# Optimization experiments

Measured on AMD Instinct MI355X. Metric: run time of the kernel, lower is better.

Reference implementation:

```python
import jax, jax.numpy as jnp
import numpy as np

SLOTS = 64
TOPK = 1
GATE_MAX = 0.2
MEM_SCALE = 0.5
DELTA_CLIP = 2.0
LN_EPS = 1e-5


def setup_inputs() -> dict:
    key = jax.random.key(0)
    ks = jax.random.split(key, 6)
    B, T, D = 8, 4096, 896
    h = jax.random.normal(ks[0], (B, T, D), dtype=jnp.float32)
    attention_mask = jnp.ones((B, T), dtype=jnp.int32)
    ln_g = jnp.ones((D,), dtype=jnp.float32)
    ln_b = jnp.zeros((D,), dtype=jnp.float32)
    W_out = (jax.random.normal(ks[1], (D, D), dtype=jnp.float32) * 0.02)      # mem_out: Linear(D,D,bias=False)
    W_nm = (jax.random.normal(ks[2], (1, 2 * D), dtype=jnp.float32) * 0.02)   # neuromod: Linear(2D,1)
    b_nm = jnp.zeros((1,), dtype=jnp.float32)
    W_wg = (jax.random.normal(ks[3], (1, D + 1), dtype=jnp.float32) * 0.02)   # write_gate: Linear(D+1,1)
    b_wg = jnp.zeros((1,), dtype=jnp.float32)
    return dict(h=h, attention_mask=attention_mask, ln_g=ln_g, ln_b=ln_b,
                W_out=W_out, W_nm=W_nm, b_nm=b_nm, W_wg=W_wg, b_wg=b_wg)


def reference(h, attention_mask, ln_g, ln_b, W_out, W_nm, b_nm, W_wg, b_wg):
    B, T, D = h.shape
    scale = 1.0 / jnp.sqrt(jnp.float32(D))
    mem_k0 = jnp.zeros((B, SLOTS, D), dtype=jnp.float32)
    mem_v0 = jnp.zeros((B, SLOTS, D), dtype=jnp.float32)
    keep = attention_mask.astype(jnp.float32)
    batch_idx = jnp.arange(B)[:, None]

    def step(carry, xs):
        mem_k, mem_v = carry
        h_t, keep_t = xs                                   # [B,D], [B]
        # content-based read: attention over slots
        scores = jnp.einsum('bd,bsd->bs', h_t, mem_k) * scale
        attn = jax.nn.softmax(scores, axis=-1)
        m = jnp.einsum('bs,bsd->bd', attn, mem_v)          # [B,D]
        # neuromodulator gate
        g = jax.nn.sigmoid(jnp.concatenate([h_t, m], axis=-1) @ W_nm.T + b_nm)   # [B,1]
        # write gate, clamped and masked by attention mask
        wg = jax.nn.sigmoid(jnp.concatenate([h_t, g], axis=-1) @ W_wg.T + b_wg)  # [B,1]
        wg = jnp.clip(wg, 0.0, GATE_MAX) * keep_t[:, None]
        # top-k gated write with straight-through selection
        soft = jax.nn.softmax(scores, axis=-1)             # address by content similarity
        _, idx = jax.lax.top_k(soft, TOPK)                 # [B,TOPK]
        hard = jnp.zeros_like(soft).at[batch_idx, idx].set(1.0 / TOPK)
        w = hard + soft - jax.lax.stop_gradient(soft)      # straight-through weights [B,S]
        gw = (wg * w)[..., None]                           # [B,S,1]
        mem_k = mem_k * (1.0 - gw) + gw * h_t[:, None, :]
        mem_v = mem_v * (1.0 - gw) + gw * h_t[:, None, :]
        # memory residual: LN -> Linear -> scale -> clip
        mu = jnp.mean(m, axis=-1, keepdims=True)
        var = jnp.var(m, axis=-1, keepdims=True)
        mn = (m - mu) / jnp.sqrt(var + LN_EPS) * ln_g + ln_b
        delta = jnp.clip((mn @ W_out.T) * MEM_SCALE, -DELTA_CLIP, DELTA_CLIP)
        return (mem_k, mem_v), h_t + delta

    xs = (jnp.swapaxes(h, 0, 1), jnp.swapaxes(keep, 0, 1))  # time-major for scan
    (_, _), h2 = jax.lax.scan(step, (mem_k0, mem_v0), xs)
    return jnp.swapaxes(h2, 0, 1)                          # [B,T,D]
```

## Files before the change

### kernel.cpp

```cpp
#include <hip/hip_runtime.h>
#include <hip/hip_bf16.h>

#define DIM 896
#define TT 4096
#define BB 8
#define NS 64
#define CC 128
#define NC 32
#define RCH 256
#define NRC 16
#define NSLICE 14

typedef float floatx4 __attribute__((ext_vector_type(4)));
typedef short short8 __attribute__((ext_vector_type(8)));

#define DPP_F(x_, ctrl_, rmask_, old_) \
  __int_as_float(__builtin_amdgcn_update_dpp(__float_as_int(old_), __float_as_int(x_), (ctrl_), (rmask_), 0xf, false))

__device__ __forceinline__ float wave_sum64(float x) {
    x += DPP_F(x, 0x111, 0xf, 0.0f);
    x += DPP_F(x, 0x112, 0xf, 0.0f);
    x += DPP_F(x, 0x114, 0xf, 0.0f);
    x += DPP_F(x, 0x118, 0xf, 0.0f);
    x += DPP_F(x, 0x142, 0xa, 0.0f);
    x += DPP_F(x, 0x143, 0xc, 0.0f);
    return __int_as_float(__builtin_amdgcn_readlane(__float_as_int(x), 63));
}
__device__ __forceinline__ float wave_max64(float x) {
    x = fmaxf(x, DPP_F(x, 0x111, 0xf, -INFINITY));
    x = fmaxf(x, DPP_F(x, 0x112, 0xf, -INFINITY));
    x = fmaxf(x, DPP_F(x, 0x114, 0xf, -INFINITY));
    x = fmaxf(x, DPP_F(x, 0x118, 0xf, -INFINITY));
    x = fmaxf(x, DPP_F(x, 0x142, 0xa, -INFINITY));
    x = fmaxf(x, DPP_F(x, 0x143, 0xc, -INFINITY));
    return __int_as_float(__builtin_amdgcn_readlane(__float_as_int(x), 63));
}

__device__ __forceinline__ float rfl_f(float x) {
    return __int_as_float(__builtin_amdgcn_readfirstlane(__float_as_int(x)));
}
__device__ __forceinline__ float rl_f(float x, int l) {
    return __int_as_float(__builtin_amdgcn_readlane(__float_as_int(x), l));
}

__global__ __launch_bounds__(64) void k0_dots(const float* __restrict__ h,
                                              const float* __restrict__ W_nm,
                                              const float* __restrict__ W_wg,
                                              float* __restrict__ R, float* __restrict__ Q,
                                              float* __restrict__ P2) {
    const int r = blockIdx.x;
    const int lane = threadIdx.x;
    const float2* hr = (const float2*)(h + (size_t)r * DIM);
    const float2* w0 = (const float2*)W_nm;
    const float2* w1 = (const float2*)(W_nm + DIM);
    const float2* w2 = (const float2*)W_wg;
    float a = 0.f, bsum = 0.f, c = 0.f;
    #pragma unroll
    for (int i = 0; i < 7; ++i) {
        int idx = lane + 64 * i;
        float2 hv = hr[idx];
        float2 a0 = w0[idx], a1 = w1[idx], a2 = w2[idx];
        a = fmaf(hv.x, a0.x, fmaf(hv.y, a0.y, a));
        bsum = fmaf(hv.x, a1.x, fmaf(hv.y, a1.y, bsum));
        c = fmaf(hv.x, a2.x, fmaf(hv.y, a2.y, c));
    }
    #pragma unroll
    for (int off = 32; off; off >>= 1) {
        a += __shfl_xor(a, off);
        bsum += __shfl_xor(bsum, off);
        c += __shfl_xor(c, off);
    }
    if (lane == 0) { R[r] = a; P2[r] = bsum; Q[r] = c; }
}

__global__ __launch_bounds__(256) void kG_gram(const float* __restrict__ h,
                                               float* __restrict__ Gd) {
    const int blk = blockIdx.x;
    const int bc = blk >> 1, half = blk & 1;
    const int b = bc / NC, c = bc % NC;
    const int tid = threadIdx.x;
    const int ti = tid >> 4, tj = tid & 15;
    __shared__ float Hs[32][132];
    float acc[8][4];
    #pragma unroll
    for (int u = 0; u < 8; u++)
        #pragma unroll
        for (int v = 0; v < 4; v++) acc[u][v] = 0.f;
    const size_t hb = (size_t)b * TT * DIM + (size_t)c * CC * DIM;
    for (int kb = 0; kb < 28; ++kb) {
        __syncthreads();
        #pragma unroll
        for (int l = 0; l < 4; ++l) {
            int idx = tid + l * 256;
            int r = idx >> 3, kq = idx & 7;
            float4 f = *(const float4*)&h[hb + (size_t)r * DIM + kb * 32 + kq * 4];
            Hs[kq * 4 + 0][r] = f.x; Hs[kq * 4 + 1][r] = f.y;
            Hs[kq * 4 + 2][r] = f.z; Hs[kq * 4 + 3][r] = f.w;
        }
        __syncthreads();
        #pragma unroll 4
        for (int k = 0; k < 32; ++k) {
            float4 a0 = *(const float4*)&Hs[k][ti * 8];
            float4 a1 = *(const float4*)&Hs[k][ti * 8 + 4];
            float4 bv = *(const float4*)&Hs[k][half * 64 + tj * 4];
            float av[8] = {a0.x, a0.y, a0.z, a0.w, a1.x, a1.y, a1.z, a1.w};
            float bb[4] = {bv.x, bv.y, bv.z, bv.w};
            #pragma unroll
            for (int u = 0; u < 8; u++)
                #pragma unroll
                for (int v = 0; v < 4; v++)
                    acc[u][v] = fmaf(av[u], bb[v], acc[u][v]);
        }
    }
    float* gp = Gd + (size_t)bc * CC * CC;
    #pragma unroll
    for (int u = 0; u < 8; u++) {
        float4 o = {acc[u][0], acc[u][1], acc[u][2], acc[u][3]};
        *(float4*)&gp[(size_t)(ti * 8 + u) * CC + half * 64 + tj * 4] = o;
    }
}

#define MC_(i) case i: mc[i] = fmaf(mc[i], om, wh); break;
__global__ __launch_bounds__(256) void kB_base(const float* __restrict__ h,
                                               const float* __restrict__ wgbuf,
                                               const int* __restrict__ ssbuf,
                                               float* __restrict__ memS,
                                               float* __restrict__ snap,
                                               float* __restrict__ Bpart,
                                               int c) {
    const int slice = blockIdx.x;
    const int b = blockIdx.y;
    const int tid = threadIdx.x;
    __shared__ float wsh[CC];
    __shared__ int   ssh[CC];
    __shared__ float Asb[64][65];
    __shared__ float Bsb[CC][65];

    if (tid < CC) {
        wsh[tid] = wgbuf[b * TT + (c - 1) * CC + tid];
        ssh[tid] = ssbuf[b * TT + (c - 1) * CC + tid];
    }
    const int q = tid >> 6, d = tid & 63;
    const int dg = slice * 64 + d;
    float mc[16];
    #pragma unroll
    for (int j = 0; j < 16; j++) mc[j] = memS[((size_t)b * NS + q * 16 + j) * DIM + dg];
    __syncthreads();

    const size_t hb = (size_t)b * TT * DIM + (size_t)((c - 1) * CC) * DIM + dg;
    float hv[16];
    #pragma unroll
    for (int j = 0; j < 16; ++j) hv[j] = h[hb + (size_t)j * DIM];
    for (int i0 = 0; i0 < CC; i0 += 16) {
        float hvn[16];
        if (i0 + 16 < CC) {
            #pragma unroll
            for (int j = 0; j < 16; ++j) hvn[j] = h[hb + (size_t)(i0 + 16 + j) * DIM];
        }
        #pragma unroll
        for (int j = 0; j < 16; ++j) {
            const int i = i0 + j;
            float hvv = hv[j];
            int ss = __builtin_amdgcn_readfirstlane(ssh[i]);
            float w = rfl_f(wsh[i]);
            if ((ss >> 4) == q) {
                float om = 1.f - w, wh = w * hvv;
                switch (ss & 15) {
                    MC_(0) MC_(1) MC_(2) MC_(3) MC_(4) MC_(5) MC_(6) MC_(7)
                    MC_(8) MC_(9) MC_(10) MC_(11) MC_(12) MC_(13) MC_(14) MC_(15)
                }
            }
        }
        #pragma unroll
        for (int j = 0; j < 16; ++j) hv[j] = hvn[j];
    }
    #pragma unroll
    for (int j = 0; j < 16; j++) {
        memS[((size_t)b * NS + q * 16 + j) * DIM + dg] = mc[j];
        Asb[d][q * 16 + j] = mc[j];
    }
    if ((c & 1) == 0) {
        const int r = c >> 1;
        #pragma unroll
        for (int j = 0; j < 16; j++)
            snap[(((size_t)b * NRC + r) * NS + q * 16 + j) * DIM + dg] = mc[j];
    }
    const size_t hb2 = (size_t)b * TT * DIM + (size_t)(c * CC) * DIM + slice * 64;
    for (int idx = tid; idx < CC * 64; idx += 256) {
        int tp = idx >> 6, k = idx & 63;
        Bsb[tp][k] = h[hb2 + (size_t)tp * DIM + k];
    }
    __syncthreads();

    const int tg = tid >> 3, sg = tid & 7;
    float acc[4][8];
    #pragma unroll
    for (int v = 0; v < 4; v++)
        #pragma unroll
        for (int u = 0; u < 8; u++) acc[v][u] = 0.f;
    #pragma unroll 4
    for (int k = 0; k < 64; ++k) {
        float bv[4], av[8];
        #pragma unroll
        for (int v = 0; v < 4; v++) bv[v] = Bsb[tg * 4 + v][k];
        #pragma unroll
        for (int u = 0; u < 8; u++) av[u] = Asb[k][sg * 8 + u];
        #pragma unroll
        for (int v = 0; v < 4; v++)
            #pragma unroll
            for (int u = 0; u < 8; u++)
                acc[v][u] = fmaf(bv[v], av[u], acc[v][u]);
    }
    float* bp = Bpart + ((size_t)(slice * BB + b)) * CC * NS;
    #pragma unroll
    for (int v = 0; v < 4; v++) {
        float4 o0 = {acc[v][0], acc[v][1], acc[v][2], acc[v][3]};
        float4 o1 = {acc[v][4], acc[v][5], acc[v][6], acc[v][7]};
        *(float4*)&bp[(size_t)(tg * 4 + v) * NS + sg * 8] = o0;
        *(float4*)&bp[(size_t)(tg * 4 + v) * NS + sg * 8 + 4] = o1;
    }
}

__global__ __launch_bounds__(256) void kS_seq(const float* __restrict__ Bpart,
                                              const float* __restrict__ Gd,
                                              const float* __restrict__ Rv,
                                              const float* __restrict__ Qv,
                                              const float* __restrict__ P2v,
                                              const int* __restrict__ mask,
                                              const float* __restrict__ b_nm,
                                              const float* __restrict__ b_wg,
                                              const float* __restrict__ W_wg,
                                              float* __restrict__ Kvec,
                                              float* __restrict__ fbuf,
                                              float* __restrict__ wgbuf,
                                              int* __restrict__ ssbuf,
                                              int c) {
    const int b = blockIdx.x;
    const int tid = threadIdx.x;
    const int lane = tid & 63;
    __shared__ float S[CC * 65];
    const int t0 = c * CC;
    const int tb = b * TT + t0;

    {
        const int w4 = tid >> 6;
        if (c == 0) {
            #pragma unroll 4
            for (int t = w4 * 32; t < w4 * 32 + 32; ++t) S[t * 65 + lane] = 0.f;
        } else {
            const float* bp0 = Bpart + (size_t)b * CC * NS;
            for (int t = w4 * 32; t < w4 * 32 + 32; ++t) {
                float s = 0.f;
                #pragma unroll
                for (int sl = 0; sl < NSLICE; ++sl)
                    s += bp0[(size_t)sl * (BB * CC * NS) + (size_t)t * NS + lane];
                S[t * 65 + lane] = s;
            }
        }
    }
    __syncthreads();
    if (tid >= 64) return;

    float Rl0 = Rv[tb + lane],  Rl1 = Rv[tb + 64 + lane];
    float Ql0 = Qv[tb + lane],  Ql1 = Qv[tb + 64 + lane];
    float Pl0 = P2v[tb + lane], Pl1 = P2v[tb + 64 + lane];
    float Ml0 = (float)mask[tb + lane], Ml1 = (float)mask[tb + 64 + lane];

    float K = Kvec[b * NS + lane];
    const float scale = 1.0f / sqrtf((float)DIM);
    const float bnm = b_nm[0], bwg = b_wg[0], wD = W_wg[DIM];
    const float* gdc = Gd + (size_t)(b * NC + c) * CC * CC;

    float g0s[4], g1s[4];
    #pragma unroll
    for (int j = 0; j < 4; ++j) {
        int r1 = j + 1 + lane, r2 = j + 65 + lane;
        g0s[j] = gdc[(size_t)j * CC + r1];
        g1s[j] = (r2 < CC) ? gdc[(size_t)j * CC + r2] : 0.f;
    }
    float cur = S[0 * 65 + lane];
    float p1 = S[1 * 65 + lane];
    float p2 = S[2 * 65 + lane];
    float p3 = S[3 * 65 + lane];

    for (int T = 0; T < CC; T += 4) {
        #pragma unroll
        for (int j = 0; j < 4; ++j) {
            const int tau = T + j;
            float p4 = (tau + 4 < CC) ? S[(tau + 4) * 65 + lane] : 0.f;
            const float g0 = g0s[j], g1 = g1s[j];
            {
                const int tn = tau + 4;
                int r1n = tn + 1 + lane, r2n = tn + 65 + lane;
                g0s[j] = (tn < CC && r1n < CC) ? gdc[(size_t)tn * CC + r1n] : 0.f;
                g1s[j] = (tn < CC && r2n < CC) ? gdc[(size_t)tn * CC + r2n] : 0.f;
            }
            const float Rt = rl_f((tau & 64) ? Rl1 : Rl0, tau & 63);
            const float Qt = rl_f((tau & 64) ? Ql1 : Ql0, tau & 63);
            const float Pt = rl_f((tau & 64) ? Pl1 : Pl0, tau & 63);
            const float Mk = rl_f((tau & 64) ? Ml1 : Ml0, tau & 63);

            float sco = cur * scale;
            float mv = wave_max64(sco);
            float e = __expf(sco);
            float se = wave_sum64(e);
            float sk = wave_sum64(e * K);
            unsigned long long bal = __ballot(sco == mv);
            int mi = (int)__ffsll(bal) - 1;

            float inv = 1.f / se;
            fbuf[((size_t)tb + tau) * NS + lane] = e * inv;
            float gdot = sk * inv;
            float g = 1.f / (1.f + __expf(-(Rt + gdot + bnm)));
            float w = 1.f / (1.f + __expf(-(Qt + g * wD + bwg)));
            w = fminf(w, 0.2f) * Mk;
            if (lane == 0) {
                wgbuf[tb + tau] = w;
                ssbuf[tb + tau] = mi;
            }
            float om = 1.f - w;
            K = (lane == mi) ? fmaf(K, om, w * Pt) : K;

            int r1 = tau + 1 + lane, r2 = tau + 65 + lane;
            if (lane >= 4 && r1 < CC) S[r1 * 65 + mi] = fmaf(S[r1 * 65 + mi], om, w * g0);
            if (r2 < CC) S[r2 * 65 + mi] = fmaf(S[r2 * 65 + mi], om, w * g1);

            const float q1 = rl_f(g0, 0), q2 = rl_f(g0, 1);
            const float q3 = rl_f(g0, 2), q4 = rl_f(g0, 3);
            const bool m_ = (lane == mi);
            p1 = m_ ? fmaf(p1, om, w * q1) : p1;
            p2 = m_ ? fmaf(p2, om, w * q2) : p2;
            p3 = m_ ? fmaf(p3, om, w * q3) : p3;
            p4 = m_ ? fmaf(p4, om, w * q4) : p4;
            cur = p1; p1 = p2; p2 = p3; p3 = p4;
        }
    }
    Kvec[b * NS + lane] = K;
}

__global__ __launch_bounds__(256) void k1_wcvt(const float* __restrict__ W,
                                               __hip_bfloat16* __restrict__ Wb) {
    const int idx = blockIdx.x * 256 + threadIdx.x;
    const float4 f = ((const float4*)W)[idx];
    alignas(8) __hip_bfloat16 t[4];
    t[0] = __float2bfloat16(f.x); t[1] = __float2bfloat16(f.y);
    t[2] = __float2bfloat16(f.z); t[3] = __float2bfloat16(f.w);
    *(uint2*)&Wb[(size_t)idx * 4] = *(const uint2*)t;
}

#define CS_(i) case i: mem[i] = fmaf(mem[i], sA, aB); break;
__global__ __launch_bounds__(448) void k2_replay(const float* __restrict__ h,
                                                 const float* __restrict__ fbuf,
                                                 const float* __restrict__ wgbuf,
                                                 const int* __restrict__ ssbuf,
                                                 const float* __restrict__ snap,
                                                 __hip_bfloat16* __restrict__ Mbuf) {
    const int blk = blockIdx.x;
    const int b = blk >> 5;
    const int c = (blk >> 1) & 15;
    const int halfD = blk & 1;
    const int tid = threadIdx.x;
    const int dg = halfD * 448 + tid;

    __shared__ float lf[128 * NS];
    __shared__ float lwg[RCH];
    __shared__ int   lss[RCH];

    float mem[64];
    const float* sp = snap + (((size_t)b * NRC + c) * NS) * DIM + dg;
    #pragma unroll
    for (int s2 = 0; s2 < 64; s2++) mem[s2] = sp[(size_t)s2 * DIM];

    const int t0 = c * RCH;
    if (tid < RCH) {
        lwg[tid] = wgbuf[b * TT + t0 + tid];
        lss[tid] = ssbuf[b * TT + t0 + tid];
    }
    const size_t hbase = (size_t)b * TT * DIM + (size_t)t0 * DIM + dg;
    const size_t fbase = ((size_t)b * TT + t0) * NS;
    const size_t mrow = ((size_t)b * TT + t0) * DIM + dg;

    for (int half = 0; half < 2; ++half) {
        __syncthreads();
        const float4* src = (const float4*)(fbuf + fbase + (size_t)half * 128 * NS);
        for (int idx = tid; idx < 128 * NS / 4; idx += 448)
            ((float4*)lf)[idx] = src[idx];
        __syncthreads();

        float hv[8];
        #pragma unroll
        for (int j = 0; j < 8; ++j)
            hv[j] = h[hbase + (size_t)(half * 128 + j) * DIM];

        for (int tg = 0; tg < 128; tg += 8) {
            float hvn[8];
            if (tg + 8 < 128) {
                #pragma unroll
                for (int j = 0; j < 8; ++j)
                    hvn[j] = h[hbase + (size_t)(half * 128 + tg + 8 + j) * DIM];
            }
// ... 19 lines not shown
                    CS_(0) CS_(1) CS_(2) CS_(3) CS_(4) CS_(5) CS_(6) CS_(7)
                    CS_(8) CS_(9) CS_(10) CS_(11) CS_(12) CS_(13) CS_(14) CS_(15)
                    CS_(16) CS_(17) CS_(18) CS_(19) CS_(20) CS_(21) CS_(22) CS_(23)
                    CS_(24) CS_(25) CS_(26) CS_(27) CS_(28) CS_(29) CS_(30) CS_(31)
                    CS_(32) CS_(33) CS_(34) CS_(35) CS_(36) CS_(37) CS_(38) CS_(39)
                    CS_(40) CS_(41) CS_(42) CS_(43) CS_(44) CS_(45) CS_(46) CS_(47)
                    CS_(48) CS_(49) CS_(50) CS_(51) CS_(52) CS_(53) CS_(54) CS_(55)
                    CS_(56) CS_(57) CS_(58) CS_(59) CS_(60) CS_(61) CS_(62) CS_(63)
                }
            }
            #pragma unroll
            for (int j = 0; j < 8; ++j) hv[j] = hvn[j];
        }
    }
}

__global__ __launch_bounds__(64) void k3_ln(__hip_bfloat16* __restrict__ Mbuf,
                                            const float* __restrict__ ln_g,
                                            const float* __restrict__ ln_b) {
    const size_t r = blockIdx.x;
    const int lane = threadIdx.x;
    __hip_bfloat162* row2 = (__hip_bfloat162*)(Mbuf + r * DIM);
    float vx[7], vy[7];
    float s1 = 0.f, s2 = 0.f;
    #pragma unroll
    for (int i = 0; i < 7; i++) {
        __hip_bfloat162 x2 = row2[lane + 64 * i];
        float x = __bfloat162float(x2.x), y = __bfloat162float(x2.y);
        vx[i] = x; vy[i] = y;
        s1 += x + y;
        s2 = fmaf(x, x, fmaf(y, y, s2));
    }
    #pragma unroll
    for (int off = 32; off; off >>= 1) {
        s1 += __shfl_xor(s1, off);
        s2 += __shfl_xor(s2, off);
    }
    float mu = s1 * (1.0f / DIM);
    float var = fmaxf(s2 * (1.0f / DIM) - mu * mu, 0.0f);
    float rs = 1.0f / sqrtf(var + 1e-5f);
    #pragma unroll
    for (int i = 0; i < 7; i++) {
        int d = 2 * (lane + 64 * i);
        float2 lg = *(const float2*)&ln_g[d];
        float2 lb = *(const float2*)&ln_b[d];
        __hip_bfloat162 o;
        o.x = __float2bfloat16((vx[i] - mu) * rs * lg.x + lb.x);
        o.y = __float2bfloat16((vy[i] - mu) * rs * lg.y + lb.y);
        row2[lane + 64 * i] = o;
    }
}

__global__ __launch_bounds__(256) void k4_gemm(const __hip_bfloat16* __restrict__ Mn,
                                               const __hip_bfloat16* __restrict__ Wb,
                                               const float* __restrict__ h,
                                               float* __restrict__ out) {
    const int nt = blockIdx.x;
    const int mt = blockIdx.y;
    const int tid = threadIdx.x;
    const int wave = tid >> 6, lane = tid & 63;
    const int wr = wave >> 1, wc = wave & 1;

    __shared__ __hip_bfloat16 Asb[128 * 72];
    __shared__ __hip_bfloat16 Bsb[128 * 72];

    floatx4 acc[4][4];
    #pragma unroll
    for (int i = 0; i < 4; i++)
        #pragma unroll
        for (int jn = 0; jn < 4; jn++)
            acc[i][jn] = (floatx4){0.f, 0.f, 0.f, 0.f};

    const int lrow = lane & 15;
    const int lk = (lane >> 4) * 8;
    const int rr = tid >> 3, ch = tid & 7;

    for (int kt = 0; kt < 14; ++kt) {
        #pragma unroll
        for (int it = 0; it < 4; ++it) {
            int row = rr + 32 * it;
            const uint4* srcA = (const uint4*)(Mn + ((size_t)(mt * 128 + row)) * DIM + kt * 64 + ch * 8);
            *(uint4*)&Asb[row * 72 + ch * 8] = *srcA;
            const uint4* srcB = (const uint4*)(Wb + ((size_t)(nt * 128 + row)) * DIM + kt * 64 + ch * 8);
            *(uint4*)&Bsb[row * 72 + ch * 8] = *srcB;
        }
        __syncthreads();
        #pragma unroll
        for (int kk = 0; kk < 2; ++kk) {
            short8 af[4], bfr[4];
            #pragma unroll
            for (int i = 0; i < 4; i++)
                af[i] = *(const short8*)&Asb[(wr * 64 + i * 16 + lrow) * 72 + kk * 32 + lk];
            #pragma unroll
            for (int i2 = 0; i2 < 4; i2++)
                bfr[i2] = *(const short8*)&Bsb[(wc * 64 + i2 * 16 + lrow) * 72 + kk * 32 + lk];
            #pragma unroll
            for (int i = 0; i < 4; i++)
                #pragma unroll
                for (int jn = 0; jn < 4; jn++)
                    acc[i][jn] = __builtin_amdgcn_mfma_f32_16x16x32_bf16(af[i], bfr[jn], acc[i][jn], 0, 0, 0);
        }
        __syncthreads();
    }
    const int crow = (lane >> 4) * 4, ccol = lane & 15;
    #pragma unroll
    for (int i = 0; i < 4; i++)
        #pragma unroll
        for (int jn = 0; jn < 4; jn++)
            #pragma unroll
            for (int rg = 0; rg < 4; rg++) {
                int rG = mt * 128 + wr * 64 + i * 16 + crow + rg;
                int nG = nt * 128 + wc * 64 + jn * 16 + ccol;
                size_t idx = (size_t)rG * DIM + nG;
                float d = acc[i][jn][rg] * 0.5f;
                d = fminf(fmaxf(d, -2.0f), 2.0f);
                out[idx] = h[idx] + d;
            }
}

extern "C" void kernel_launch(void* const* d_in, const int* in_sizes, int n_in,
                              void* d_out, int out_size, void* d_ws, size_t ws_size,
                              hipStream_t stream) {
    const float* h      = (const float*)d_in[0];
    const int* mask     = (const int*)d_in[1];
    const float* ln_g   = (const float*)d_in[2];
    const float* ln_b   = (const float*)d_in[3];
    const float* W_out  = (const float*)d_in[4];
    const float* W_nm   = (const float*)d_in[5];
    const float* b_nm   = (const float*)d_in[6];
    const float* W_wg   = (const float*)d_in[7];
    const float* b_wg   = (const float*)d_in[8];
    float* out = (float*)d_out;

    char* ws = (char*)d_ws;
    float* Bpart = (float*)(ws);
    float* memS  = (float*)(ws + 8388608);
    float* Kvec  = (float*)(ws + 8388608 + 1835008);
    float* snap  = (float*)(ws + 8388608 + 1835008 + 2048);
    const size_t Z0 = 8388608;
    const size_t ZBYTES = 1835008 + 2048 + 29360128;
    float* fbuf  = (float*)(ws + 8388608 + ZBYTES);
    float* wgbuf = (float*)(ws + 8388608 + ZBYTES + 8388608);
    int*   ssbuf = (int*)  (ws + 8388608 + ZBYTES + 8388608 + 131072);
    char*  Mreg  = ws + 8388608 + ZBYTES + 8388608 + 262144;
    float* Gd = (float*)(Mreg);
    float* R  = (float*)(Mreg + 16777216);
    float* Q  = (float*)(Mreg + 16777216 + 131072);
    float* P2 = (float*)(Mreg + 16777216 + 262144);
    __hip_bfloat16* Mbuf = (__hip_bfloat16*)Mreg;
    __hip_bfloat16* Wb = (__hip_bfloat16*)(ws);

    hipMemsetAsync(ws + Z0, 0, ZBYTES, stream);
    hipLaunchKernelGGL(k0_dots, dim3(BB * TT), dim3(64), 0, stream,
                       h, W_nm, W_wg, R, Q, P2);
    hipLaunchKernelGGL(kG_gram, dim3(BB * NC * 2), dim3(256), 0, stream, h, Gd);

    hipLaunchKernelGGL(kS_seq, dim3(BB), dim3(256), 0, stream,
                       Bpart, Gd, R, Q, P2, mask, b_nm, b_wg, W_wg,
                       Kvec, fbuf, wgbuf, ssbuf, 0);
    for (int c = 1; c < NC; ++c) {
        hipLaunchKernelGGL(kB_base, dim3(NSLICE, BB), dim3(256), 0, stream,
                           h, wgbuf, ssbuf, memS, snap, Bpart, c);
        hipLaunchKernelGGL(kS_seq, dim3(BB), dim3(256), 0, stream,
                           Bpart, Gd, R, Q, P2, mask, b_nm, b_wg, W_wg,
                           Kvec, fbuf, wgbuf, ssbuf, c);
    }

    hipLaunchKernelGGL(k1_wcvt, dim3(784), dim3(256), 0, stream, W_out, Wb);
    hipLaunchKernelGGL(k2_replay, dim3(BB * NRC * 2), dim3(448), 0, stream,
                       h, fbuf, wgbuf, ssbuf, snap, Mbuf);
    hipLaunchKernelGGL(k3_ln, dim3(BB * TT), dim3(64), 0, stream,
                       Mbuf, ln_g, ln_b);
    hipLaunchKernelGGL(k4_gemm, dim3(7, 256), dim3(256), 0, stream,
                       Mbuf, Wb, h, out);
}
```

Baseline: 4.320 ms.

## Double chunk size to halve sequential launches and fold weight conversion into GEMM

Raises the chunk length from 128 to 256 steps, halving the number of serialized kB_base/kS_seq launch pairs. The Gram kernel now computes the 256x256 per-chunk Gram from three 128x128 tiles (the symmetric lower block is skipped) and uses a skewed shared-memory layout. The sequential kernel keeps four register-carried rows and holds a larger S array in shared memory, so each kS_seq call does twice the serial work. The separate W_out bf16 conversion kernel is removed and the conversion happens inside the GEMM tile load instead, which repeats the conversion work across blocks.

```diff
diff --git a/kernel.cpp b/kernel.cpp
--- a/kernel.cpp
+++ b/kernel.cpp
@@ -5,8 +5,8 @@
 #define TT 4096
 #define BB 8
 #define NS 64
-#define CC 128
-#define NC 32
+#define CC 256
+#define NC 16
 #define RCH 256
 #define NRC 16
 #define NSLICE 14
@@ -73,50 +73,69 @@
     if (lane == 0) { R[r] = a; P2[r] = bsum; Q[r] = c; }
 }
 
+#define KSW(cx) ((cx) + (((cx) >> 5) << 2))
 __global__ __launch_bounds__(256) void kG_gram(const float* __restrict__ h,
                                                float* __restrict__ Gd) {
     const int blk = blockIdx.x;
-    const int bc = blk >> 1, half = blk & 1;
+    const int bc = blk / 3, pair = blk % 3;
     const int b = bc / NC, c = bc % NC;
+    const int rh = (pair == 2) ? 1 : 0;
+    const int ch2 = (pair >= 1) ? 1 : 0;
     const int tid = threadIdx.x;
     const int ti = tid >> 4, tj = tid & 15;
-    __shared__ float Hs[32][132];
-    float acc[8][4];
+    __shared__ float Ar[32 * 140];
+    __shared__ float Ac[32 * 140];
+    float acc[8][8];
     #pragma unroll
     for (int u = 0; u < 8; u++)
         #pragma unroll
-        for (int v = 0; v < 4; v++) acc[u][v] = 0.f;
-    const size_t hb = (size_t)b * TT * DIM + (size_t)c * CC * DIM;
+        for (int v = 0; v < 8; v++) acc[u][v] = 0.f;
+    const size_t hbR = (size_t)b * TT * DIM + (size_t)(c * CC + rh * 128) * DIM;
+    const size_t hbC = (size_t)b * TT * DIM + (size_t)(c * CC + ch2 * 128) * DIM;
+    const float* Acp = (pair == 1) ? Ac : Ar;
+    const int cbr = ti * 8 + ((ti >> 2) << 2);
+    const int cbc = tj * 8 + ((tj >> 2) << 2);
     for (int kb = 0; kb < 28; ++kb) {
         __syncthreads();
         #pragma unroll
         for (int l = 0; l < 4; ++l) {
             int idx = tid + l * 256;
             int r = idx >> 3, kq = idx & 7;
-            float4 f = *(const float4*)&h[hb + (size_t)r * DIM + kb * 32 + kq * 4];
-            Hs[kq * 4 + 0][r] = f.x; Hs[kq * 4 + 1][r] = f.y;
-            Hs[kq * 4 + 2][r] = f.z; Hs[kq * 4 + 3][r] = f.w;
+            int rs = KSW(r);
+            float4 f = *(const float4*)&h[hbR + (size_t)r * DIM + kb * 32 + kq * 4];
+            Ar[(kq * 4 + 0) * 140 + rs] = f.x; Ar[(kq * 4 + 1) * 140 + rs] = f.y;
+            Ar[(kq * 4 + 2) * 140 + rs] = f.z; Ar[(kq * 4 + 3) * 140 + rs] = f.w;
+            if (pair == 1) {
+                float4 g = *(const float4*)&h[hbC + (size_t)r * DIM + kb * 32 + kq * 4];
+                Ac[(kq * 4 + 0) * 140 + rs] = g.x; Ac[(kq * 4 + 1) * 140 + rs] = g.y;
+                Ac[(kq * 4 + 2) * 140 + rs] = g.z; Ac[(kq * 4 + 3) * 140 + rs] = g.w;
+            }
         }
         __syncthreads();
         #pragma unroll 4
         for (int k = 0; k < 32; ++k) {
-            float4 a0 = *(const float4*)&Hs[k][ti * 8];
-            float4 a1 = *(const float4*)&Hs[k][ti * 8 + 4];
-            float4 bv = *(const float4*)&Hs[k][half * 64 + tj * 4];
+            float4 a0 = *(const float4*)&Ar[k * 140 + cbr];
+            float4 a1 = *(const float4*)&Ar[k * 140 + cbr + 4];
+            float4 b0 = *(const float4*)&Acp[k * 140 + cbc];
+            float4 b1 = *(const float4*)&Acp[k * 140 + cbc + 4];
             float av[8] = {a0.x, a0.y, a0.z, a0.w, a1.x, a1.y, a1.z, a1.w};
-            float bb[4] = {bv.x, bv.y, bv.z, bv.w};
+            float bv[8] = {b0.x, b0.y, b0.z, b0.w, b1.x, b1.y, b1.z, b1.w};
             #pragma unroll
             for (int u = 0; u < 8; u++)
                 #pragma unroll
-                for (int v = 0; v < 4; v++)
-                    acc[u][v] = fmaf(av[u], bb[v], acc[u][v]);
+                for (int v = 0; v < 8; v++)
+                    acc[u][v] = fmaf(av[u], bv[v], acc[u][v]);
         }
     }
     float* gp = Gd + (size_t)bc * CC * CC;
     #pragma unroll
     for (int u = 0; u < 8; u++) {
-        float4 o = {acc[u][0], acc[u][1], acc[u][2], acc[u][3]};
-        *(float4*)&gp[(size_t)(ti * 8 + u) * CC + half * 64 + tj * 4] = o;
+        int row = rh * 128 + ti * 8 + u;
+        int col = ch2 * 128 + tj * 8;
+        float4 o0 = {acc[u][0], acc[u][1], acc[u][2], acc[u][3]};
+        float4 o1 = {acc[u][4], acc[u][5], acc[u][6], acc[u][7]};
+        *(float4*)&gp[(size_t)row * CC + col] = o0;
+        *(float4*)&gp[(size_t)row * CC + col + 4] = o1;
     }
 }
 
@@ -134,12 +153,10 @@
     __shared__ float wsh[CC];
     __shared__ int   ssh[CC];
     __shared__ float Asb[64][65];
-    __shared__ float Bsb[CC][65];
-
-    if (tid < CC) {
-        wsh[tid] = wgbuf[b * TT + (c - 1) * CC + tid];
-        ssh[tid] = ssbuf[b * TT + (c - 1) * CC + tid];
-    }
+    __shared__ float Bsb[128][65];
+
+    wsh[tid] = wgbuf[b * TT + (c - 1) * CC + tid];
+    ssh[tid] = ssbuf[b * TT + (c - 1) * CC + tid];
     const int q = tid >> 6, d = tid & 63;
     const int dg = slice * 64 + d;
     float mc[16];
@@ -179,45 +196,45 @@
         memS[((size_t)b * NS + q * 16 + j) * DIM + dg] = mc[j];
         Asb[d][q * 16 + j] = mc[j];
     }
-    if ((c & 1) == 0) {
-        const int r = c >> 1;
-        #pragma unroll
-        for (int j = 0; j < 16; j++)
-            snap[(((size_t)b * NRC + r) * NS + q * 16 + j) * DIM + dg] = mc[j];
-    }
-    const size_t hb2 = (size_t)b * TT * DIM + (size_t)(c * CC) * DIM + slice * 64;
-    for (int idx = tid; idx < CC * 64; idx += 256) {
-        int tp = idx >> 6, k = idx & 63;
-        Bsb[tp][k] = h[hb2 + (size_t)tp * DIM + k];
-    }
-    __syncthreads();
+    #pragma unroll
+    for (int j = 0; j < 16; j++)
+        snap[(((size_t)b * NRC + c) * NS + q * 16 + j) * DIM + dg] = mc[j];
 
     const int tg = tid >> 3, sg = tid & 7;
-    float acc[4][8];
-    #pragma unroll
-    for (int v = 0; v < 4; v++)
-        #pragma unroll
-        for (int u = 0; u < 8; u++) acc[v][u] = 0.f;
-    #pragma unroll 4
-    for (int k = 0; k < 64; ++k) {
-        float bv[4], av[8];
-        #pragma unroll
-        for (int v = 0; v < 4; v++) bv[v] = Bsb[tg * 4 + v][k];
-        #pragma unroll
-        for (int u = 0; u < 8; u++) av[u] = Asb[k][sg * 8 + u];
+    float* bp = Bpart + ((size_t)(slice * BB + b)) * CC * NS;
+    for (int hf = 0; hf < 2; ++hf) {
+        __syncthreads();
+        const size_t hb2 = (size_t)b * TT * DIM + (size_t)(c * CC + hf * 128) * DIM + slice * 64;
+        for (int idx = tid; idx < 128 * 64; idx += 256) {
+            int tp = idx >> 6, k = idx & 63;
+            Bsb[tp][k] = h[hb2 + (size_t)tp * DIM + k];
+        }
+        __syncthreads();
+        float acc[4][8];
         #pragma unroll
         for (int v = 0; v < 4; v++)
             #pragma unroll
-            for (int u = 0; u < 8; u++)
-                acc[v][u] = fmaf(bv[v], av[u], acc[v][u]);
-    }
-    float* bp = Bpart + ((size_t)(slice * BB + b)) * CC * NS;
-    #pragma unroll
-    for (int v = 0; v < 4; v++) {
-        float4 o0 = {acc[v][0], acc[v][1], acc[v][2], acc[v][3]};
-        float4 o1 = {acc[v][4], acc[v][5], acc[v][6], acc[v][7]};
-        *(float4*)&bp[(size_t)(tg * 4 + v) * NS + sg * 8] = o0;
-        *(float4*)&bp[(size_t)(tg * 4 + v) * NS + sg * 8 + 4] = o1;
+            for (int u = 0; u < 8; u++) acc[v][u] = 0.f;
+        #pragma unroll 4
+        for (int k = 0; k < 64; ++k) {
+            float bv[4], av[8];
+            #pragma unroll
+            for (int v = 0; v < 4; v++) bv[v] = Bsb[tg * 4 + v][k];
+            #pragma unroll
+            for (int u = 0; u < 8; u++) av[u] = Asb[k][sg * 8 + u];
+            #pragma unroll
+            for (int v = 0; v < 4; v++)
+                #pragma unroll
+                for (int u = 0; u < 8; u++)
+                    acc[v][u] = fmaf(bv[v], av[u], acc[v][u]);
+        }
+        #pragma unroll
+        for (int v = 0; v < 4; v++) {
+            float4 o0 = {acc[v][0], acc[v][1], acc[v][2], acc[v][3]};
+            float4 o1 = {acc[v][4], acc[v][5], acc[v][6], acc[v][7]};
+            *(float4*)&bp[(size_t)(hf * 128 + tg * 4 + v) * NS + sg * 8] = o0;
+            *(float4*)&bp[(size_t)(hf * 128 + tg * 4 + v) * NS + sg * 8 + 4] = o1;
+        }
     }
 }
 
@@ -238,67 +255,94 @@
     const int b = blockIdx.x;
     const int tid = threadIdx.x;
     const int lane = tid & 63;
-    __shared__ float S[CC * 65];
+    __shared__ float S[252 * 65];
     const int t0 = c * CC;
     const int tb = b * TT + t0;
-
-    {
+    const float* bp0 = Bpart + (size_t)b * CC * NS;
+
+    if (c == 0) {
         const int w4 = tid >> 6;
-        if (c == 0) {
-            #pragma unroll 4
-            for (int t = w4 * 32; t < w4 * 32 + 32; ++t) S[t * 65 + lane] = 0.f;
-        } else {
-            const float* bp0 = Bpart + (size_t)b * CC * NS;
-            for (int t = w4 * 32; t < w4 * 32 + 32; ++t) {
-                float s = 0.f;
-                #pragma unroll
-                for (int sl = 0; sl < NSLICE; ++sl)
-                    s += bp0[(size_t)sl * (BB * CC * NS) + (size_t)t * NS + lane];
-                S[t * 65 + lane] = s;
-            }
+        for (int t = 4 + w4 * 63; t < 4 + w4 * 63 + 63 && t < 256; ++t) S[(t - 4) * 65 + lane] = 0.f;
+        for (int t = 4 + 252 + tid; t < 256; t += 256) S[(t - 4) * 65 + lane] = 0.f;
+    } else {
+        const int quad = tid & 15;
+        const int g16 = tid >> 4;
+        for (int t = 4 + g16; t < 256; t += 16) {
+            float s0 = 0.f, s1 = 0.f, s2 = 0.f, s3 = 0.f;
+            #pragma unroll
+            for (int sl = 0; sl < NSLICE; ++sl) {
+                float4 v = *(const float4*)&bp0[(size_t)sl * (BB * CC * NS) + (size_t)t * NS + quad * 4];
+                s0 += v.x; s1 += v.y; s2 += v.z; s3 += v.w;
+            }
+            S[(t - 4) * 65 + quad * 4 + 0] = s0;
+            S[(t - 4) * 65 + quad * 4 + 1] = s1;
+            S[(t - 4) * 65 + quad * 4 + 2] = s2;
+            S[(t - 4) * 65 + quad * 4 + 3] = s3;
         }
     }
     __syncthreads();
     if (tid >= 64) return;
 
-    float Rl0 = Rv[tb + lane],  Rl1 = Rv[tb + 64 + lane];
-    float Ql0 = Qv[tb + lane],  Ql1 = Qv[tb + 64 + lane];
-    float Pl0 = P2v[tb + lane], Pl1 = P2v[tb + 64 + lane];
-    float Ml0 = (float)mask[tb + lane], Ml1 = (float)mask[tb + 64 + lane];
+    float cur, p1, p2, p3;
+    if (c == 0) { cur = p1 = p2 = p3 = 0.f; }
+    else {
+        float c0 = 0.f, c1 = 0.f, c2 = 0.f, c3 = 0.f;
+        #pragma unroll
+        for (int sl = 0; sl < NSLICE; ++sl) {
+            const float* p = bp0 + (size_t)sl * (BB * CC * NS);
+            c0 += p[lane]; c1 += p[64 + lane]; c2 += p[128 + lane]; c3 += p[192 + lane];
+        }
+        cur = c0; p1 = c1; p2 = c2; p3 = c3;
+    }
+
+    float Rl0 = Rv[tb + lane],       Rl1 = Rv[tb + 64 + lane];
+    float Rl2 = Rv[tb + 128 + lane], Rl3 = Rv[tb + 192 + lane];
+    float Ql0 = Qv[tb + lane],       Ql1 = Qv[tb + 64 + lane];
+    float Ql2 = Qv[tb + 128 + lane], Ql3 = Qv[tb + 192 + lane];
+    float Pl0 = P2v[tb + lane],      Pl1 = P2v[tb + 64 + lane];
+    float Pl2 = P2v[tb + 128 + lane],Pl3 = P2v[tb + 192 + lane];
+    float Ml0 = (float)mask[tb + lane],       Ml1 = (float)mask[tb + 64 + lane];
+    float Ml2 = (float)mask[tb + 128 + lane], Ml3 = (float)mask[tb + 192 + lane];
 
     float K = Kvec[b * NS + lane];
     const float scale = 1.0f / sqrtf((float)DIM);
     const float bnm = b_nm[0], bwg = b_wg[0], wD = W_wg[DIM];
     const float* gdc = Gd + (size_t)(b * NC + c) * CC * CC;
 
-    float g0s[4], g1s[4];
+    float g0s[4], g1s[4], g2s[4], g3s[4];
     #pragma unroll
     for (int j = 0; j < 4; ++j) {
-        int r1 = j + 1 + lane, r2 = j + 65 + lane;
+        int r1 = j + 1 + lane, r2 = j + 65 + lane, r3 = j + 129 + lane, r4 = j + 193 + lane;
         g0s[j] = gdc[(size_t)j * CC + r1];
-        g1s[j] = (r2 < CC) ? gdc[(size_t)j * CC + r2] : 0.f;
-    }
-    float cur = S[0 * 65 + lane];
-    float p1 = S[1 * 65 + lane];
-    float p2 = S[2 * 65 + lane];
-    float p3 = S[3 * 65 + lane];
+        g1s[j] = gdc[(size_t)j * CC + r2];
+        g2s[j] = gdc[(size_t)j * CC + r3];
+        g3s[j] = (r4 < CC) ? gdc[(size_t)j * CC + r4] : 0.f;
+    }
 
     for (int T = 0; T < CC; T += 4) {
         #pragma unroll
         for (int j = 0; j < 4; ++j) {
             const int tau = T + j;
-            float p4 = (tau + 4 < CC) ? S[(tau + 4) * 65 + lane] : 0.f;
-            const float g0 = g0s[j], g1 = g1s[j];
+            float p4 = (tau + 4 < CC) ? S[tau * 65 + lane] : 0.f;
+            const float g0 = g0s[j], g1 = g1s[j], g2 = g2s[j], g3 = g3s[j];
             {
                 const int tn = tau + 4;
                 int r1n = tn + 1 + lane, r2n = tn + 65 + lane;
+                int r3n = tn + 129 + lane, r4n = tn + 193 + lane;
                 g0s[j] = (tn < CC && r1n < CC) ? gdc[(size_t)tn * CC + r1n] : 0.f;
                 g1s[j] = (tn < CC && r2n < CC) ? gdc[(size_t)tn * CC + r2n] : 0.f;
-            }
-            const float Rt = rl_f((tau & 64) ? Rl1 : Rl0, tau & 63);
-            const float Qt = rl_f((tau & 64) ? Ql1 : Ql0, tau & 63);
-            const float Pt = rl_f((tau & 64) ? Pl1 : Pl0, tau & 63);
-            const float Mk = rl_f((tau & 64) ? Ml1 : Ml0, tau & 63);
+                g2s[j] = (tn < CC && r3n < CC) ? gdc[(size_t)tn * CC + r3n] : 0.f;
+                g3s[j] = (tn < CC && r4n < CC) ? gdc[(size_t)tn * CC + r4n] : 0.f;
+            }
+            const int t6a = (tau >> 7) & 1, t6b = (tau >> 6) & 1;
+            float Rsel = t6a ? (t6b ? Rl3 : Rl2) : (t6b ? Rl1 : Rl0);
+            float Qsel = t6a ? (t6b ? Ql3 : Ql2) : (t6b ? Ql1 : Ql0);
+            float Psel = t6a ? (t6b ? Pl3 : Pl2) : (t6b ? Pl1 : Pl0);
+            float Msel = t6a ? (t6b ? Ml3 : Ml2) : (t6b ? Ml1 : Ml0);
+            const float Rt = rl_f(Rsel, tau & 63);
+            const float Qt = rl_f(Qsel, tau & 63);
+            const float Pt = rl_f(Psel, tau & 63);
+            const float Mk = rl_f(Msel, tau & 63);
 
             float sco = cur * scale;
             float mv = wave_max64(sco);
@@ -322,8 +366,11 @@
             K = (lane == mi) ? fmaf(K, om, w * Pt) : K;
 
             int r1 = tau + 1 + lane, r2 = tau + 65 + lane;
-            if (lane >= 4 && r1 < CC) S[r1 * 65 + mi] = fmaf(S[r1 * 65 + mi], om, w * g0);
-            if (r2 < CC) S[r2 * 65 + mi] = fmaf(S[r2 * 65 + mi], om, w * g1);
+            int r3 = tau + 129 + lane, r4 = tau + 193 + lane;
+            if (lane >= 4 && r1 < CC) S[(r1 - 4) * 65 + mi] = fmaf(S[(r1 - 4) * 65 + mi], om, w * g0);
+            if (r2 < CC) S[(r2 - 4) * 65 + mi] = fmaf(S[(r2 - 4) * 65 + mi], om, w * g1);
+            if (r3 < CC) S[(r3 - 4) * 65 + mi] = fmaf(S[(r3 - 4) * 65 + mi], om, w * g2);
+            if (r4 < CC) S[(r4 - 4) * 65 + mi] = fmaf(S[(r4 - 4) * 65 + mi], om, w * g3);
 
             const float q1 = rl_f(g0, 0), q2 = rl_f(g0, 1);
             const float q3 = rl_f(g0, 2), q4 = rl_f(g0, 3);
@@ -336,16 +383,6 @@
         }
     }
     Kvec[b * NS + lane] = K;
-}
-
-__global__ __launch_bounds__(256) void k1_wcvt(const float* __restrict__ W,
-                                               __hip_bfloat16* __restrict__ Wb) {
-    const int idx = blockIdx.x * 256 + threadIdx.x;
-    const float4 f = ((const float4*)W)[idx];
-    alignas(8) __hip_bfloat16 t[4];
-    t[0] = __float2bfloat16(f.x); t[1] = __float2bfloat16(f.y);
-    t[2] = __float2bfloat16(f.z); t[3] = __float2bfloat16(f.w);
-    *(uint2*)&Wb[(size_t)idx * 4] = *(const uint2*)t;
 }
 
 #define CS_(i) case i: mem[i] = fmaf(mem[i], sA, aB); break;
@@ -471,7 +508,7 @@
 }
 
 __global__ __launch_bounds__(256) void k4_gemm(const __hip_bfloat16* __restrict__ Mn,
-                                               const __hip_bfloat16* __restrict__ Wb,
+                                               const float* __restrict__ W_out,
                                                const float* __restrict__ h,
                                                float* __restrict__ out) {
     const int nt = blockIdx.x;
@@ -500,8 +537,15 @@
             int row = rr + 32 * it;
             const uint4* srcA = (const uint4*)(Mn + ((size_t)(mt * 128 + row)) * DIM + kt * 64 + ch * 8);
             *(uint4*)&Asb[row * 72 + ch * 8] = *srcA;
-            const uint4* srcB = (const uint4*)(Wb + ((size_t)(nt * 128 + row)) * DIM + kt * 64 + ch * 8);
-            *(uint4*)&Bsb[row * 72 + ch * 8] = *srcB;
+            const float* srcB = W_out + ((size_t)(nt * 128 + row)) * DIM + kt * 64 + ch * 8;
+            float4 f0 = *(const float4*)srcB;
+            float4 f1 = *(const float4*)(srcB + 4);
+            alignas(16) __hip_bfloat16 tmp[8];
+            tmp[0] = __float2bfloat16(f0.x); tmp[1] = __float2bfloat16(f0.y);
+            tmp[2] = __float2bfloat16(f0.z); tmp[3] = __float2bfloat16(f0.w);
+            tmp[4] = __float2bfloat16(f1.x); tmp[5] = __float2bfloat16(f1.y);
+            tmp[6] = __float2bfloat16(f1.z); tmp[7] = __float2bfloat16(f1.w);
+            *(uint4*)&Bsb[row * 72 + ch * 8] = *(uint4*)tmp;
         }
         __syncthreads();
         #pragma unroll
@@ -553,26 +597,25 @@
 
     char* ws = (char*)d_ws;
     float* Bpart = (float*)(ws);
-    float* memS  = (float*)(ws + 8388608);
-    float* Kvec  = (float*)(ws + 8388608 + 1835008);
-    float* snap  = (float*)(ws + 8388608 + 1835008 + 2048);
-    const size_t Z0 = 8388608;
+    float* memS  = (float*)(ws + 7340032);
+    float* Kvec  = (float*)(ws + 7340032 + 1835008);
+    float* snap  = (float*)(ws + 7340032 + 1835008 + 2048);
+    const size_t ZOFF = 7340032;
     const size_t ZBYTES = 1835008 + 2048 + 29360128;
-    float* fbuf  = (float*)(ws + 8388608 + ZBYTES);
-    float* wgbuf = (float*)(ws + 8388608 + ZBYTES + 8388608);
-    int*   ssbuf = (int*)  (ws + 8388608 + ZBYTES + 8388608 + 131072);
-    char*  Mreg  = ws + 8388608 + ZBYTES + 8388608 + 262144;
+    float* fbuf  = (float*)(ws + 38537216);
+    float* wgbuf = (float*)(ws + 46925824);
+    int*   ssbuf = (int*)  (ws + 47056896);
+    char*  Mreg  = ws + 47187968;
     float* Gd = (float*)(Mreg);
-    float* R  = (float*)(Mreg + 16777216);
-    float* Q  = (float*)(Mreg + 16777216 + 131072);
-    float* P2 = (float*)(Mreg + 16777216 + 262144);
+    float* R  = (float*)(Mreg + 33554432);
+    float* Q  = (float*)(Mreg + 33554432 + 131072);
+    float* P2 = (float*)(Mreg + 33554432 + 262144);
     __hip_bfloat16* Mbuf = (__hip_bfloat16*)Mreg;
-    __hip_bfloat16* Wb = (__hip_bfloat16*)(ws);
-
-    hipMemsetAsync(ws + Z0, 0, ZBYTES, stream);
+
+    hipMemsetAsync(ws + ZOFF, 0, ZBYTES, stream);
     hipLaunchKernelGGL(k0_dots, dim3(BB * TT), dim3(64), 0, stream,
                        h, W_nm, W_wg, R, Q, P2);
-    hipLaunchKernelGGL(kG_gram, dim3(BB * NC * 2), dim3(256), 0, stream, h, Gd);
+    hipLaunchKernelGGL(kG_gram, dim3(BB * NC * 3), dim3(256), 0, stream, h, Gd);
 
     hipLaunchKernelGGL(kS_seq, dim3(BB), dim3(256), 0, stream,
                        Bpart, Gd, R, Q, P2, mask, b_nm, b_wg, W_wg,
@@ -585,11 +628,10 @@
                            Kvec, fbuf, wgbuf, ssbuf, c);
     }
 
-    hipLaunchKernelGGL(k1_wcvt, dim3(784), dim3(256), 0, stream, W_out, Wb);
     hipLaunchKernelGGL(k2_replay, dim3(BB * NRC * 2), dim3(448), 0, stream,
                        h, fbuf, wgbuf, ssbuf, snap, Mbuf);
     hipLaunchKernelGGL(k3_ln, dim3(BB * TT), dim3(64), 0, stream,
                        Mbuf, ln_g, ln_b);
     hipLaunchKernelGGL(k4_gemm, dim3(7, 256), dim3(256), 0, stream,
-                       Mbuf, Wb, h, out);
-}
+                       Mbuf, W_out, h, out);
+}
```

After: 4.404 ms. About the same (+2.0%).

## Speculatively precompute next-step softmax reductions before the slot update

Applied to the files above, without the earlier changes.

Restructures the serial per-timestep recurrence so the wave reductions (max, sum of exp, weighted sum) for the next step are computed from the pre-update scores. They are then patched with a scalar correction for the single slot that gets written. This takes the cross-lane reductions off the critical dependency chain between the gate computation and the next step's argmax. The cost is extra exp and reduction work per step, and the incremental sum correction may introduce small floating-point differences.

```diff
diff --git a/kernel.cpp b/kernel.cpp
--- a/kernel.cpp
+++ b/kernel.cpp
@@ -278,16 +278,27 @@
         g0s[j] = gdc[(size_t)j * CC + r1];
         g1s[j] = (r2 < CC) ? gdc[(size_t)j * CC + r2] : 0.f;
     }
-    float cur = S[0 * 65 + lane];
     float p1 = S[1 * 65 + lane];
     float p2 = S[2 * 65 + lane];
     float p3 = S[3 * 65 + lane];
 
+    float e, se, sk; int mi;
+    {
+        float cur = S[0 * 65 + lane];
+        float sco = cur * scale;
+        float mv = wave_max64(sco);
+        e  = __expf(sco);
+        se = wave_sum64(e);
+        sk = wave_sum64(e * K);
+        unsigned long long bal = __ballot(sco == mv);
+        mi = (int)__ffsll(bal) - 1;
+    }
+
     for (int T = 0; T < CC; T += 4) {
         #pragma unroll
         for (int j = 0; j < 4; ++j) {
             const int tau = T + j;
-            float p4 = (tau + 4 < CC) ? S[(tau + 4) * 65 + lane] : 0.f;
+            float p4 = (tau + 4 < CC) ? S[tau * 65 + 260 + lane] : 0.f;
             const float g0 = g0s[j], g1 = g1s[j];
             {
                 const int tn = tau + 4;
@@ -300,13 +311,16 @@
             const float Pt = rl_f((tau & 64) ? Pl1 : Pl0, tau & 63);
             const float Mk = rl_f((tau & 64) ? Ml1 : Ml0, tau & 63);
 
-            float sco = cur * scale;
-            float mv = wave_max64(sco);
-            float e = __expf(sco);
-            float se = wave_sum64(e);
-            float sk = wave_sum64(e * K);
-            unsigned long long bal = __ballot(sco == mv);
-            int mi = (int)__ffsll(bal) - 1;
+            float pm = (lane == mi) ? -INFINITY : p1;
+            float mx1 = wave_max64(pm);
+            unsigned long long b1 = __ballot(pm == mx1);
+            int ax1 = (int)__ffsll(b1) - 1;
+            float e1s = __expf(p1 * scale);
+            float se1 = wave_sum64(e1s);
+            float sk1 = wave_sum64(e1s * K);
+            float e1old_mi = rl_f(e1s, mi);
+            float p1old_mi = rl_f(p1, mi);
+            float Kold_mi  = rl_f(K, mi);
 
             float inv = 1.f / se;
             fbuf[((size_t)tb + tau) * NS + lane] = e * inv;
@@ -319,20 +333,30 @@
                 ssbuf[tb + tau] = mi;
             }
             float om = 1.f - w;
-            K = (lane == mi) ? fmaf(K, om, w * Pt) : K;
+
+            float Knew_mi = fmaf(Kold_mi, om, w * Pt);
+            K = (lane == mi) ? Knew_mi : K;
 
             int r1 = tau + 1 + lane, r2 = tau + 65 + lane;
             if (lane >= 4 && r1 < CC) S[r1 * 65 + mi] = fmaf(S[r1 * 65 + mi], om, w * g0);
             if (r2 < CC) S[r2 * 65 + mi] = fmaf(S[r2 * 65 + mi], om, w * g1);
 
-            const float q1 = rl_f(g0, 0), q2 = rl_f(g0, 1);
-            const float q3 = rl_f(g0, 2), q4 = rl_f(g0, 3);
+            const float gself = rl_f(g0, 0);
+            const float q2 = rl_f(g0, 1), q3 = rl_f(g0, 2), q4 = rl_f(g0, 3);
+            float s1new = fmaf(p1old_mi, om, w * gself);
             const bool m_ = (lane == mi);
-            p1 = m_ ? fmaf(p1, om, w * q1) : p1;
+            p1 = m_ ? s1new : p1;
             p2 = m_ ? fmaf(p2, om, w * q2) : p2;
             p3 = m_ ? fmaf(p3, om, w * q3) : p3;
             p4 = m_ ? fmaf(p4, om, w * q4) : p4;
-            cur = p1; p1 = p2; p2 = p3; p3 = p4;
+
+            float e1new = __expf(s1new * scale);
+            se = se1 - e1old_mi + e1new;
+            sk = sk1 - e1old_mi * Kold_mi + e1new * Knew_mi;
+            e  = m_ ? e1new : e1s;
+            mi = (s1new > mx1) ? mi : ((s1new == mx1) ? (mi < ax1 ? mi : ax1) : ax1);
+
+            p1 = p2; p2 = p3; p3 = p4;
         }
     }
     Kvec[b * NS + lane] = K;
```

Measured after the change: 4.697 ms. +8.7%, slower.

## Stage Gd rows through double-buffered LDS with producer waves and XOR-swizzle S

Applied to the files above, without the earlier changes.

The sequential scan kernel now keeps its three otherwise idle waves alive and has them prefetch 16-row blocks of the Gd chunk into a double-buffered shared-memory tile. Wave 0 reads from that tile instead of issuing global loads inside the serial recurrence. The S scratch layout also changes from padded stride 65 to an XOR-swizzled 64-wide layout. The aim is to take global load latency off the critical serial path, at the cost of a block-wide barrier every 16 steps and extra LDS.

```diff
diff --git a/kernel.cpp b/kernel.cpp
--- a/kernel.cpp
+++ b/kernel.cpp
@@ -221,6 +221,7 @@
     }
 }
 
+#define SIDX(r, c_) ((((r) << 6)) + (((c_) ^ ((r) & 63))))
 __global__ __launch_bounds__(256) void kS_seq(const float* __restrict__ Bpart,
                                               const float* __restrict__ Gd,
                                               const float* __restrict__ Rv,
@@ -238,104 +239,124 @@
     const int b = blockIdx.x;
     const int tid = threadIdx.x;
     const int lane = tid & 63;
-    __shared__ float S[CC * 65];
+    const int wv = tid >> 6;
+    __shared__ float S[CC * 64];
+    __shared__ float Gb[2][16 * 128];
     const int t0 = c * CC;
     const int tb = b * TT + t0;
-
-    {
-        const int w4 = tid >> 6;
-        if (c == 0) {
+    const float* gdc = Gd + (size_t)(b * NC + c) * CC * CC;
+
+    if (c == 0) {
+        for (int t = wv * 32; t < wv * 32 + 32; ++t) S[SIDX(t, lane)] = 0.f;
+    } else {
+        const float* bp0 = Bpart + (size_t)b * CC * NS;
+        for (int t = wv * 32; t < wv * 32 + 32; ++t) {
+            float s = 0.f;
+            #pragma unroll
+            for (int sl = 0; sl < NSLICE; ++sl)
+                s += bp0[(size_t)sl * (BB * CC * NS) + (size_t)t * NS + lane];
+            S[SIDX(t, lane)] = s;
+        }
+    }
+    for (int idx = tid; idx < 512; idx += 256) {
+        int r = idx >> 5, cq = idx & 31;
+        *(float4*)&Gb[0][r * 128 + cq * 4] = *(const float4*)&gdc[(size_t)r * CC + cq * 4];
+    }
+
+    float cur = 0.f, p1 = 0.f, p2 = 0.f, p3 = 0.f, K = 0.f;
+    float Rl0 = 0.f, Rl1 = 0.f, Ql0 = 0.f, Ql1 = 0.f;
+    float Pl0 = 0.f, Pl1 = 0.f, Ml0 = 0.f, Ml1 = 0.f;
+    float bnm = 0.f, bwg = 0.f, wD = 0.f;
+    const float scale = 1.0f / sqrtf((float)DIM);
+    if (wv == 0) {
+        cur = S[SIDX(0, lane)];
+        p1  = S[SIDX(1, lane)];
+        p2  = S[SIDX(2, lane)];
+        p3  = S[SIDX(3, lane)];
+        K = Kvec[b * NS + lane];
+        Rl0 = Rv[tb + lane];  Rl1 = Rv[tb + 64 + lane];
+        Ql0 = Qv[tb + lane];  Ql1 = Qv[tb + 64 + lane];
+        Pl0 = P2v[tb + lane]; Pl1 = P2v[tb + 64 + lane];
+        Ml0 = (float)mask[tb + lane]; Ml1 = (float)mask[tb + 64 + lane];
+        bnm = b_nm[0]; bwg = b_wg[0]; wD = W_wg[DIM];
+    }
+    __syncthreads();
+
+    for (int bb = 0; bb < 8; ++bb) {
+        if (wv == 0) {
+            const int base = bb * 16;
+            const float* gcur = Gb[bb & 1];
+            int c0 = base + 1 + lane, c1 = base + 65 + lane;
+            float g0 = (c0 < CC) ? gcur[c0] : 0.f;
+            float g1 = (c1 < CC) ? gcur[c1] : 0.f;
             #pragma unroll 4
-            for (int t = w4 * 32; t < w4 * 32 + 32; ++t) S[t * 65 + lane] = 0.f;
-        } else {
-            const float* bp0 = Bpart + (size_t)b * CC * NS;
-            for (int t = w4 * 32; t < w4 * 32 + 32; ++t) {
-                float s = 0.f;
-                #pragma unroll
-                for (int sl = 0; sl < NSLICE; ++sl)
-                    s += bp0[(size_t)sl * (BB * CC * NS) + (size_t)t * NS + lane];
-                S[t * 65 + lane] = s;
+            for (int s = 0; s < 16; ++s) {
+                const int tau = base + s;
+                float g0n = 0.f, g1n = 0.f;
+                if (s < 15) {
+                    int r1n = tau + 2 + lane, r2n = tau + 66 + lane;
+                    if (r1n < CC) g0n = gcur[(s + 1) * 128 + r1n];
+                    if (r2n < CC) g1n = gcur[(s + 1) * 128 + r2n];
+                }
+                float p4 = (tau + 4 < CC) ? S[SIDX(tau + 4, lane)] : 0.f;
+                const float Rt = rl_f((tau & 64) ? Rl1 : Rl0, tau & 63);
+                const float Qt = rl_f((tau & 64) ? Ql1 : Ql0, tau & 63);
+                const float Pt = rl_f((tau & 64) ? Pl1 : Pl0, tau & 63);
+                const float Mk = rl_f((tau & 64) ? Ml1 : Ml0, tau & 63);
+
+                float sco = cur * scale;
+                float mv = wave_max64(sco);
+                float e = __expf(sco);
+                float se = wave_sum64(e);
+                float sk = wave_sum64(e * K);
+                unsigned long long bal = __ballot(sco == mv);
+                int mi = (int)__ffsll(bal) - 1;
+
+                float inv = 1.f / se;
+                fbuf[((size_t)tb + tau) * NS + lane] = e * inv;
+                float gdot = sk * inv;
+                float g = 1.f / (1.f + __expf(-(Rt + gdot + bnm)));
+                float w = 1.f / (1.f + __expf(-(Qt + g * wD + bwg)));
+                w = fminf(w, 0.2f) * Mk;
+                if (lane == 0) {
+                    wgbuf[tb + tau] = w;
+                    ssbuf[tb + tau] = mi;
+                }
+                float om = 1.f - w;
+                K = (lane == mi) ? fmaf(K, om, w * Pt) : K;
+
+                int r1 = tau + 1 + lane, r2 = tau + 65 + lane;
+                if (lane >= 4 && r1 < CC) {
+                    int ix = SIDX(r1, mi);
+                    S[ix] = fmaf(S[ix], om, w * g0);
+                }
+                if (r2 < CC) {
+                    int ix2 = SIDX(r2, mi);
+                    S[ix2] = fmaf(S[ix2], om, w * g1);
+                }
+
+                const float q1 = rl_f(g0, 0), q2 = rl_f(g0, 1);
+                const float q3 = rl_f(g0, 2), q4 = rl_f(g0, 3);
+                const bool m_ = (lane == mi);
+                p1 = m_ ? fmaf(p1, om, w * q1) : p1;
+                p2 = m_ ? fmaf(p2, om, w * q2) : p2;
+                p3 = m_ ? fmaf(p3, om, w * q3) : p3;
+                p4 = m_ ? fmaf(p4, om, w * q4) : p4;
+                cur = p1; p1 = p2; p2 = p3; p3 = p4;
+                g0 = g0n; g1 = g1n;
             }
-        }
-    }
-    __syncthreads();
-    if (tid >= 64) return;
-
-    float Rl0 = Rv[tb + lane],  Rl1 = Rv[tb + 64 + lane];
-    float Ql0 = Qv[tb + lane],  Ql1 = Qv[tb + 64 + lane];
-    float Pl0 = P2v[tb + lane], Pl1 = P2v[tb + 64 + lane];
-    float Ml0 = (float)mask[tb + lane], Ml1 = (float)mask[tb + 64 + lane];
-
-    float K = Kvec[b * NS + lane];
-    const float scale = 1.0f / sqrtf((float)DIM);
-    const float bnm = b_nm[0], bwg = b_wg[0], wD = W_wg[DIM];
-    const float* gdc = Gd + (size_t)(b * NC + c) * CC * CC;
-
-    float g0s[4], g1s[4];
-    #pragma unroll
-    for (int j = 0; j < 4; ++j) {
-        int r1 = j + 1 + lane, r2 = j + 65 + lane;
-        g0s[j] = gdc[(size_t)j * CC + r1];
-        g1s[j] = (r2 < CC) ? gdc[(size_t)j * CC + r2] : 0.f;
-    }
-    float cur = S[0 * 65 + lane];
-    float p1 = S[1 * 65 + lane];
-    float p2 = S[2 * 65 + lane];
-    float p3 = S[3 * 65 + lane];
-
-    for (int T = 0; T < CC; T += 4) {
-        #pragma unroll
-        for (int j = 0; j < 4; ++j) {
-            const int tau = T + j;
-            float p4 = (tau + 4 < CC) ? S[(tau + 4) * 65 + lane] : 0.f;
-            const float g0 = g0s[j], g1 = g1s[j];
-            {
-                const int tn = tau + 4;
-                int r1n = tn + 1 + lane, r2n = tn + 65 + lane;
-                g0s[j] = (tn < CC && r1n < CC) ? gdc[(size_t)tn * CC + r1n] : 0.f;
-                g1s[j] = (tn < CC && r2n < CC) ? gdc[(size_t)tn * CC + r2n] : 0.f;
+        } else if (bb < 7) {
+            const int bs = (bb + 1) * 16;
+            float* dst = Gb[(bb + 1) & 1];
+            for (int idx = tid - 64; idx < 512; idx += 192) {
+                int r = idx >> 5, cq = idx & 31;
+                *(float4*)&dst[r * 128 + cq * 4] =
+                    *(const float4*)&gdc[(size_t)(bs + r) * CC + cq * 4];
             }
-            const float Rt = rl_f((tau & 64) ? Rl1 : Rl0, tau & 63);
-            const float Qt = rl_f((tau & 64) ? Ql1 : Ql0, tau & 63);
-            const float Pt = rl_f((tau & 64) ? Pl1 : Pl0, tau & 63);
-            const float Mk = rl_f((tau & 64) ? Ml1 : Ml0, tau & 63);
-
-            float sco = cur * scale;
-            float mv = wave_max64(sco);
-            float e = __expf(sco);
-            float se = wave_sum64(e);
-            float sk = wave_sum64(e * K);
-            unsigned long long bal = __ballot(sco == mv);
-            int mi = (int)__ffsll(bal) - 1;
-
-            float inv = 1.f / se;
-            fbuf[((size_t)tb + tau) * NS + lane] = e * inv;
-            float gdot = sk * inv;
-            float g = 1.f / (1.f + __expf(-(Rt + gdot + bnm)));
-            float w = 1.f / (1.f + __expf(-(Qt + g * wD + bwg)));
-            w = fminf(w, 0.2f) * Mk;
-            if (lane == 0) {
-                wgbuf[tb + tau] = w;
-                ssbuf[tb + tau] = mi;
-            }
-            float om = 1.f - w;
-            K = (lane == mi) ? fmaf(K, om, w * Pt) : K;
-
-            int r1 = tau + 1 + lane, r2 = tau + 65 + lane;
-            if (lane >= 4 && r1 < CC) S[r1 * 65 + mi] = fmaf(S[r1 * 65 + mi], om, w * g0);
-            if (r2 < CC) S[r2 * 65 + mi] = fmaf(S[r2 * 65 + mi], om, w * g1);
-
-            const float q1 = rl_f(g0, 0), q2 = rl_f(g0, 1);
-            const float q3 = rl_f(g0, 2), q4 = rl_f(g0, 3);
-            const bool m_ = (lane == mi);
-            p1 = m_ ? fmaf(p1, om, w * q1) : p1;
-            p2 = m_ ? fmaf(p2, om, w * q2) : p2;
-            p3 = m_ ? fmaf(p3, om, w * q3) : p3;
-            p4 = m_ ? fmaf(p4, om, w * q4) : p4;
-            cur = p1; p1 = p2; p2 = p3; p3 = p4;
-        }
-    }
-    Kvec[b * NS + lane] = K;
+        }
+        __syncthreads();
+    }
+    if (wv == 0) Kvec[b * NS + lane] = K;
 }
 
 __global__ __launch_bounds__(256) void k1_wcvt(const float* __restrict__ W,
```

Result: faster. 4.110 ms (-4.9%).
